# Performance work log

Measured on AMD Instinct MI355X. Metric: run time of the kernel, lower is better.

Reference implementation:

```python
import jax, jax.numpy as jnp
import numpy as np

N_NODES = 100000
K_HOPS = 10
ALPHA = 0.1


def gcn_conv(x, src, dst, W, b, num_nodes):
    # GCNConv: linear first (cheaper: out_dim small), then D^-1/2 (A+I) D^-1/2 aggregation
    h = x @ W  # [N, out]
    deg = jax.ops.segment_sum(jnp.ones_like(dst, dtype=h.dtype), dst, num_segments=num_nodes)
    dinv = jnp.where(deg > 0, jax.lax.rsqrt(deg), 0.0)
    norm = dinv[src] * dinv[dst]  # [E]
    msg = h[src] * norm[:, None]
    out = jax.ops.segment_sum(msg, dst, num_segments=num_nodes)
    return out + b


def _with_self_loops(edge_index, num_nodes):
    loops = jnp.arange(num_nodes, dtype=edge_index.dtype)
    src = jnp.concatenate([edge_index[0], loops])
    dst = jnp.concatenate([edge_index[1], loops])
    return src, dst


def setup_inputs() -> dict:
    key = jax.random.key(0)
    ks = jax.random.split(key, 8)
    n_feat, hidden, n_cls, n_edges = 512, 16, 7, 3200000
    x = jax.random.normal(ks[0], (N_NODES, n_feat), dtype=jnp.float32)
    edge_index = jax.random.randint(ks[1], (2, n_edges), 0, N_NODES, dtype=jnp.int64)
    W1 = jax.random.normal(ks[2], (n_feat, hidden), dtype=jnp.float32) * 0.05
    b1 = jnp.zeros((hidden,), dtype=jnp.float32)
    Wl = jax.random.normal(ks[3], (hidden, hidden), dtype=jnp.float32) * 0.25
    bl = jnp.zeros((hidden,), dtype=jnp.float32)
    W2 = jax.random.normal(ks[4], (hidden, n_cls), dtype=jnp.float32) * 0.25
    b2 = jnp.zeros((n_cls,), dtype=jnp.float32)
    return {"x": x, "edge_index": edge_index, "W1": W1, "b1": b1, "Wl": Wl, "bl": bl, "W2": W2, "b2": b2}


def reference(x, edge_index, W1, b1, Wl, bl, W2, b2):
    src, dst = _with_self_loops(edge_index, N_NODES)
    h = jax.nn.relu(gcn_conv(x, src, dst, W1, b1, N_NODES))
    def body(h, _):
        h = ALPHA * jax.nn.relu(h @ Wl + bl) + (1.0 - ALPHA) * h
        return h, None
    h, _ = jax.lax.scan(body, h, None, length=K_HOPS)
    out = gcn_conv(h, src, dst, W2, b2, N_NODES)
    return jax.nn.log_softmax(out, axis=1)
```

## Files before the change

### kernel.cpp

```cpp
#include <hip/hip_runtime.h>
#include <math.h>

#define N_NODES 100000
#define N_EDGES 3200000
#define F_IN    512
#define HID     16
#define NCLS    7
#define ALPHA   0.1f
#define K_HOPS  10

#define SHIFT   7
#define BWIDTH  128
#define NBUCK   ((N_NODES + BWIDTH - 1) / BWIDTH)
#define CHUNK   8192
#define A3_BLOCKS ((N_EDGES + CHUNK - 1) / CHUNK)

#define OFF_BCNT    0u
#define OFF_BSTART  1024u
#define OFF_BCUR    2048u
#define OFF_RP      3072u
#define OFF_DINV    103424u
#define OFF_COL     203776u
#define OFF_BINNED  3403776u
#define OFF_H0      3403776u
#define OFF_H1      5003776u
#define OFF_Z       6603776u

__global__ void k_bhist(const int* __restrict__ dst, int* __restrict__ bcnt) {
    __shared__ int h[NBUCK];
    int tid = threadIdx.x;
    for (int i = tid; i < NBUCK; i += 256) h[i] = 0;
    __syncthreads();
    for (int e = blockIdx.x * 256 + tid; e < N_EDGES; e += gridDim.x * 256)
        atomicAdd(&h[dst[e] >> SHIFT], 1);
    __syncthreads();
    for (int i = tid; i < NBUCK; i += 256) {
        int v = h[i];
        if (v) atomicAdd(&bcnt[i], v);
    }
}

__global__ void k_bscan(const int* __restrict__ bcnt, int* __restrict__ bstart,
                        int* __restrict__ bcur) {
    __shared__ int s[1024];
    int tid = threadIdx.x;
    int v = (tid < NBUCK) ? bcnt[tid] : 0;
    s[tid] = v;
    __syncthreads();
    for (int off = 1; off < 1024; off <<= 1) {
        int t = (tid >= off) ? s[tid - off] : 0;
        __syncthreads();
        s[tid] += t;
        __syncthreads();
    }
    if (tid < NBUCK) {
        int ex = s[tid] - v;
        bstart[tid] = ex;
        bcur[tid] = ex;
    }
    if (tid == 0) bstart[NBUCK] = N_EDGES;
}

__global__ void k_bin(const int* __restrict__ src, const int* __restrict__ dst,
                      int* __restrict__ bcur, unsigned int* __restrict__ binned) {
    __shared__ int ha[1024];
    __shared__ int hb[1024];
    __shared__ int gbase[NBUCK];
    __shared__ int lcur[NBUCK];
    int tid = threadIdx.x;
    int e0 = blockIdx.x * CHUNK;
    int e1 = e0 + CHUNK;
    if (e1 > N_EDGES) e1 = N_EDGES;
    for (int i = tid; i < 1024; i += 256) ha[i] = 0;
    __syncthreads();
    for (int e = e0 + tid; e < e1; e += 256)
        atomicAdd(&ha[dst[e] >> SHIFT], 1);
    __syncthreads();
    int* a = ha;
    int* b = hb;
    for (int off = 1; off < 1024; off <<= 1) {
        for (int s = tid; s < 1024; s += 256)
            b[s] = a[s] + ((s >= off) ? a[s - off] : 0);
        __syncthreads();
        int* t = a; a = b; b = t;
    }
    for (int s = tid; s < NBUCK; s += 256) {
        int c = a[s] - ((s > 0) ? a[s - 1] : 0);
        lcur[s] = 0;
        gbase[s] = c ? atomicAdd(&bcur[s], c) : 0;
    }
    __syncthreads();
    for (int e = e0 + tid; e < e1; e += 256) {
        int d = dst[e];
        int bk = d >> SHIFT;
        int idx = atomicAdd(&lcur[bk], 1);
        binned[gbase[bk] + idx] =
            ((unsigned int)(d & (BWIDTH - 1)) << 17) | (unsigned int)src[e];
    }
}

__global__ void k_csr(const unsigned int* __restrict__ binned, const int* __restrict__ bstart,
                      int* __restrict__ rp, float* __restrict__ dinv, int* __restrict__ col) {
    __shared__ int cnt[BWIDTH];
    __shared__ int s[BWIDTH];
    __shared__ int cur[BWIDTH];
    int tid = threadIdx.x;
    int b = blockIdx.x;
    int base = b << SHIFT;
    int e0 = bstart[b], e1 = bstart[b + 1];
    if (tid < BWIDTH) cnt[tid] = 0;
    __syncthreads();
    for (int e = e0 + tid; e < e1; e += 256)
        atomicAdd(&cnt[binned[e] >> 17], 1);
    __syncthreads();
    int v = 0;
    if (tid < BWIDTH) { v = cnt[tid]; s[tid] = v; }
    __syncthreads();
    for (int off = 1; off < BWIDTH; off <<= 1) {
        int t = 0;
        if (tid < BWIDTH && tid >= off) t = s[tid - off];
        __syncthreads();
        if (tid < BWIDTH) s[tid] += t;
        __syncthreads();
    }
    if (tid < BWIDTH) {
        int ex = s[tid] - v;
        cur[tid] = ex;
        int node = base + tid;
        if (node < N_NODES) {
            rp[node] = e0 + ex;
            dinv[node] = rsqrtf((float)(v + 1));
        }
    }
    if (b == 0 && tid == 0) rp[N_NODES] = N_EDGES;
    __syncthreads();
    for (int e = e0 + tid; e < e1; e += 256) {
        unsigned int w = binned[e];
        int ln = (int)(w >> 17);
        int p = atomicAdd(&cur[ln], 1);
        col[e0 + p] = (int)(w & 0x1FFFFu);
    }
}

#define XW_ROWS 64
#define XW_KT   32
#define XW_S    65
#define XW_NT   (F_IN / XW_KT)
__global__ void k_xw1(const float* __restrict__ x, const float* __restrict__ W,
                      const float* __restrict__ dinv, float* __restrict__ h0s) {
    __shared__ float xT[2][XW_KT * XW_S];
    int tid = threadIdx.x;
    int rowBase = blockIdx.x * XW_ROWS;

    int rf0 = tid >> 3, kq = tid & 7;
    int rf1 = rf0 + 32;
    bool v0 = (rowBase + rf0) < N_NODES;
    bool v1 = (rowBase + rf1) < N_NODES;
    const float* xrow0 = x + (size_t)(rowBase + rf0) * F_IN;
    const float* xrow1 = x + (size_t)(rowBase + rf1) * F_IN;

    int r  = tid & 63;
    int cg = __builtin_amdgcn_readfirstlane(tid >> 6);
    const float4* W4 = (const float4*)W;

    float4 zero4 = make_float4(0.f, 0.f, 0.f, 0.f);
    float4 acc = zero4;
    float4 ld0 = v0 ? ((const float4*)xrow0)[kq] : zero4;
    float4 ld1 = v1 ? ((const float4*)xrow1)[kq] : zero4;

    for (int kt = 0; kt < XW_NT; kt++) {
        int buf = kt & 1;
        float* xb = xT[buf];
        int kb = kq * 4;
        xb[(kb + 0) * XW_S + rf0] = ld0.x;
        xb[(kb + 1) * XW_S + rf0] = ld0.y;
        xb[(kb + 2) * XW_S + rf0] = ld0.z;
        xb[(kb + 3) * XW_S + rf0] = ld0.w;
        xb[(kb + 0) * XW_S + rf1] = ld1.x;
        xb[(kb + 1) * XW_S + rf1] = ld1.y;
        xb[(kb + 2) * XW_S + rf1] = ld1.z;
        xb[(kb + 3) * XW_S + rf1] = ld1.w;
        if (kt + 1 < XW_NT) {
            const float4* p0 = (const float4*)(xrow0 + (kt + 1) * XW_KT);
            const float4* p1 = (const float4*)(xrow1 + (kt + 1) * XW_KT);
            ld0 = v0 ? p0[kq] : zero4;
            ld1 = v1 ? p1[kq] : zero4;
        }
        __syncthreads();
        const float* xr = &xb[r];
#pragma unroll
        for (int k = 0; k < XW_KT; k++) {
            float xv = xr[k * XW_S];
            float4 w4 = W4[(kt * XW_KT + k) * 4 + cg];
            acc.x += xv * w4.x;
            acc.y += xv * w4.y;
            acc.z += xv * w4.z;
            acc.w += xv * w4.w;
        }
    }
    int node = rowBase + r;
    if (node < N_NODES) {
        float dv = dinv[node];
        float4 o;
        o.x = dv * acc.x; o.y = dv * acc.y; o.z = dv * acc.z; o.w = dv * acc.w;
        ((float4*)h0s)[(size_t)node * 4 + cg] = o;
    }
}

__global__ void k_agg1(const float* __restrict__ h0s, const int* __restrict__ rp,
                       const int* __restrict__ col, const float* __restrict__ dinv,
                       const float* __restrict__ b1, float* __restrict__ h1) {
    int node = (blockIdx.x * blockDim.x + threadIdx.x) >> 6;
    if (node >= N_NODES) return;
    int lane = threadIdx.x & 63;
    int c = lane & 15, eo = lane >> 4;
    int e0 = rp[node], e1 = rp[node + 1];
    float acc = 0.f;
    for (int e = e0 + eo; e < e1; e += 4)
        acc += h0s[(size_t)col[e] * HID + c];
    acc += __shfl_xor(acc, 16);
    acc += __shfl_xor(acc, 32);
    float o = dinv[node] * (acc + h0s[(size_t)node * HID + c]) + b1[c];
    if (eo == 0) h1[(size_t)node * HID + c] = fmaxf(o, 0.f);
}

__global__ void k_hops(const float* __restrict__ h1, const float* __restrict__ Wl,
                       const float* __restrict__ bl, const float* __restrict__ W2,
                       const float* __restrict__ dinv, float* __restrict__ zs) {
    int node = blockIdx.x * blockDim.x + threadIdx.x;
    if (node >= N_NODES) return;
    float h[HID];
    const float4* h4 = (const float4*)(h1 + (size_t)node * HID);
#pragma unroll
    for (int q = 0; q < HID / 4; q++) {
        float4 v = h4[q];
        h[q * 4 + 0] = v.x; h[q * 4 + 1] = v.y;
        h[q * 4 + 2] = v.z; h[q * 4 + 3] = v.w;
    }
    for (int it = 0; it < K_HOPS; it++) {
        float tm[HID];
#pragma unroll
        for (int c = 0; c < HID; c++) tm[c] = bl[c];
#pragma unroll
        for (int k = 0; k < HID; k++) {
            float hk = h[k];
#pragma unroll
            for (int c = 0; c < HID; c++) tm[c] += hk * Wl[k * HID + c];
        }
#pragma unroll
        for (int c = 0; c < HID; c++)
            h[c] = ALPHA * fmaxf(tm[c], 0.f) + (1.f - ALPHA) * h[c];
    }
    float dv = dinv[node];
    float zz[8];
#pragma unroll
    for (int c = 0; c < 8; c++) zz[c] = 0.f;
#pragma unroll
    for (int k = 0; k < HID; k++) {
        float hk = h[k];
#pragma unroll
        for (int c = 0; c < NCLS; c++) zz[c] += hk * W2[k * NCLS + c];
    }
    float4* z4 = (float4*)(zs + (size_t)node * 8);
    float4 v0, v1;
    v0.x = dv * zz[0]; v0.y = dv * zz[1]; v0.z = dv * zz[2]; v0.w = dv * zz[3];
    v1.x = dv * zz[4]; v1.y = dv * zz[5]; v1.z = dv * zz[6]; v1.w = 0.f;
    z4[0] = v0; z4[1] = v1;
}

__global__ void k_agg2(const float* __restrict__ zs, const int* __restrict__ rp,
                       const int* __restrict__ col, const float* __restrict__ dinv,
                       const float* __restrict__ b2, float* __restrict__ out) {
    int node = (blockIdx.x * blockDim.x + threadIdx.x) >> 6;
    if (node >= N_NODES) return;
    int lane = threadIdx.x & 63;
    int c = lane & 7, eo = lane >> 3;
    int e0 = rp[node], e1 = rp[node + 1];
    float acc = 0.f;
    for (int e = e0 + eo; e < e1; e += 8)
        acc += zs[(size_t)col[e] * 8 + c];
    acc += __shfl_xor(acc, 8);
    acc += __shfl_xor(acc, 16);
    acc += __shfl_xor(acc, 32);
    float o = dinv[node] * (acc + zs[(size_t)node * 8 + c]) + ((c < NCLS) ? b2[c] : 0.f);
    float val = (c < NCLS) ? o : -INFINITY;
    float m = val;
    m = fmaxf(m, __shfl_xor(m, 1));
    m = fmaxf(m, __shfl_xor(m, 2));
    m = fmaxf(m, __shfl_xor(m, 4));
    float ex = (c < NCLS) ? expf(o - m) : 0.f;
    float ss = ex;
    ss += __shfl_xor(ss, 1);
    ss += __shfl_xor(ss, 2);
    ss += __shfl_xor(ss, 4);
    if (eo == 0 && c < NCLS) out[(size_t)node * NCLS + c] = o - m - logf(ss);
}

extern "C" void kernel_launch(void* const* d_in, const int* in_sizes, int n_in,
                              void* d_out, int out_size, void* d_ws, size_t ws_size,
                              hipStream_t stream) {
    const float* x  = (const float*)d_in[0];
    const int*   ei = (const int*)d_in[1];
    const float* W1 = (const float*)d_in[2];
    const float* b1 = (const float*)d_in[3];
    const float* Wl = (const float*)d_in[4];
    const float* bl = (const float*)d_in[5];
    const float* W2 = (const float*)d_in[6];
    const float* b2 = (const float*)d_in[7];
    float* out = (float*)d_out;

    int*   wsI = (int*)d_ws;
    float* wsF = (float*)d_ws;
    int*          bcnt   = wsI + OFF_BCNT;
    int*          bstart = wsI + OFF_BSTART;
    int*          bcur   = wsI + OFF_BCUR;
    int*          rp     = wsI + OFF_RP;
    float*        dinv   = wsF + OFF_DINV;
    int*          col    = wsI + OFF_COL;
    unsigned int* binned = (unsigned int*)(wsI + OFF_BINNED);
    float*        h0s    = wsF + OFF_H0;
    float*        h1     = wsF + OFF_H1;
    float*        zs     = wsF + OFF_Z;

    const int* src = ei;
    const int* dst = ei + N_EDGES;

    hipMemsetAsync(bcnt, 0, NBUCK * sizeof(int), stream);

    k_bhist<<<1024, 256, 0, stream>>>(dst, bcnt);
    k_bscan<<<1, 1024, 0, stream>>>(bcnt, bstart, bcur);
    k_bin<<<A3_BLOCKS, 256, 0, stream>>>(src, dst, bcur, binned);
    k_csr<<<NBUCK, 256, 0, stream>>>(binned, bstart, rp, dinv, col);
    k_xw1<<<(N_NODES + XW_ROWS - 1) / XW_ROWS, 256, 0, stream>>>(x, W1, dinv, h0s);
    k_agg1<<<(N_NODES * 64 + 255) / 256, 256, 0, stream>>>(h0s, rp, col, dinv, b1, h1);
    k_hops<<<(N_NODES + 255) / 256, 256, 0, stream>>>(h1, Wl, bl, W2, dinv, zs);
    k_agg2<<<(N_NODES * 64 + 255) / 256, 256, 0, stream>>>(zs, rp, col, dinv, b2, out);
}
```

Baseline: 609.7 us.

## Drop full CSR build; aggregate per destination bucket with shared-memory atomics

Removes the second-level CSR construction (per-node row pointers and column array). The degree kernel now only computes dinv, and both aggregation kernels process a 128-node bucket per block, accumulating source features into a shared-memory tile with LDS atomics straight from the bucket-binned edge list. The binning kernel also caches dst values in registers and drops its 1024-entry prefix scan, since only per-bucket counts are needed. This saves one pass over the edge array and the col writes, but floating-point summation order becomes nondeterministic and LDS atomic contention on hot nodes may add cost.

Result: slower. 970.2 us (+59.1%).

```diff
diff --git a/kernel.cpp b/kernel.cpp
--- a/kernel.cpp
+++ b/kernel.cpp
@@ -13,18 +13,17 @@
 #define BWIDTH  128
 #define NBUCK   ((N_NODES + BWIDTH - 1) / BWIDTH)
 #define CHUNK   8192
+#define EPT     (CHUNK / 256)
 #define A3_BLOCKS ((N_EDGES + CHUNK - 1) / CHUNK)
 
 #define OFF_BCNT    0u
 #define OFF_BSTART  1024u
 #define OFF_BCUR    2048u
-#define OFF_RP      3072u
-#define OFF_DINV    103424u
-#define OFF_COL     203776u
-#define OFF_BINNED  3403776u
-#define OFF_H0      3403776u
-#define OFF_H1      5003776u
-#define OFF_Z       6603776u
+#define OFF_DINV    3072u
+#define OFF_BINNED  103424u
+#define OFF_H0      3303424u
+#define OFF_H1      4903424u
+#define OFF_Z       6503424u
 
 __global__ void k_bhist(const int* __restrict__ dst, int* __restrict__ bcnt) {
     __shared__ int h[NBUCK];
@@ -63,82 +62,57 @@
 
 __global__ void k_bin(const int* __restrict__ src, const int* __restrict__ dst,
                       int* __restrict__ bcur, unsigned int* __restrict__ binned) {
-    __shared__ int ha[1024];
-    __shared__ int hb[1024];
+    __shared__ int ha[NBUCK];
     __shared__ int gbase[NBUCK];
     __shared__ int lcur[NBUCK];
     int tid = threadIdx.x;
     int e0 = blockIdx.x * CHUNK;
     int e1 = e0 + CHUNK;
     if (e1 > N_EDGES) e1 = N_EDGES;
-    for (int i = tid; i < 1024; i += 256) ha[i] = 0;
-    __syncthreads();
-    for (int e = e0 + tid; e < e1; e += 256)
-        atomicAdd(&ha[dst[e] >> SHIFT], 1);
-    __syncthreads();
-    int* a = ha;
-    int* b = hb;
-    for (int off = 1; off < 1024; off <<= 1) {
-        for (int s = tid; s < 1024; s += 256)
-            b[s] = a[s] + ((s >= off) ? a[s - off] : 0);
-        __syncthreads();
-        int* t = a; a = b; b = t;
-    }
+    for (int i = tid; i < NBUCK; i += 256) ha[i] = 0;
+    __syncthreads();
+    int dloc[EPT];
+#pragma unroll
+    for (int i = 0; i < EPT; i++) {
+        int e = e0 + tid + i * 256;
+        dloc[i] = (e < e1) ? dst[e] : -1;
+        if (dloc[i] >= 0) atomicAdd(&ha[dloc[i] >> SHIFT], 1);
+    }
+    __syncthreads();
     for (int s = tid; s < NBUCK; s += 256) {
-        int c = a[s] - ((s > 0) ? a[s - 1] : 0);
+        int c = ha[s];
         lcur[s] = 0;
         gbase[s] = c ? atomicAdd(&bcur[s], c) : 0;
     }
     __syncthreads();
-    for (int e = e0 + tid; e < e1; e += 256) {
-        int d = dst[e];
-        int bk = d >> SHIFT;
-        int idx = atomicAdd(&lcur[bk], 1);
-        binned[gbase[bk] + idx] =
-            ((unsigned int)(d & (BWIDTH - 1)) << 17) | (unsigned int)src[e];
-    }
-}
-
-__global__ void k_csr(const unsigned int* __restrict__ binned, const int* __restrict__ bstart,
-                      int* __restrict__ rp, float* __restrict__ dinv, int* __restrict__ col) {
+#pragma unroll
+    for (int i = 0; i < EPT; i++) {
+        int d = dloc[i];
+        if (d >= 0) {
+            int e = e0 + tid + i * 256;
+            int bk = d >> SHIFT;
+            int idx = atomicAdd(&lcur[bk], 1);
+            binned[gbase[bk] + idx] =
+                ((unsigned int)(d & (BWIDTH - 1)) << 17) | (unsigned int)src[e];
+        }
+    }
+}
+
+__global__ void k_deg(const unsigned int* __restrict__ binned, const int* __restrict__ bstart,
+                      float* __restrict__ dinv) {
     __shared__ int cnt[BWIDTH];
-    __shared__ int s[BWIDTH];
-    __shared__ int cur[BWIDTH];
     int tid = threadIdx.x;
     int b = blockIdx.x;
     int base = b << SHIFT;
+    if (tid < BWIDTH) cnt[tid] = 0;
+    __syncthreads();
     int e0 = bstart[b], e1 = bstart[b + 1];
-    if (tid < BWIDTH) cnt[tid] = 0;
-    __syncthreads();
     for (int e = e0 + tid; e < e1; e += 256)
         atomicAdd(&cnt[binned[e] >> 17], 1);
     __syncthreads();
-    int v = 0;
-    if (tid < BWIDTH) { v = cnt[tid]; s[tid] = v; }
-    __syncthreads();
-    for (int off = 1; off < BWIDTH; off <<= 1) {
-        int t = 0;
-        if (tid < BWIDTH && tid >= off) t = s[tid - off];
-        __syncthreads();
-        if (tid < BWIDTH) s[tid] += t;
-        __syncthreads();
-    }
     if (tid < BWIDTH) {
-        int ex = s[tid] - v;
-        cur[tid] = ex;
         int node = base + tid;
-        if (node < N_NODES) {
-            rp[node] = e0 + ex;
-            dinv[node] = rsqrtf((float)(v + 1));
-        }
-    }
-    if (b == 0 && tid == 0) rp[N_NODES] = N_EDGES;
-    __syncthreads();
-    for (int e = e0 + tid; e < e1; e += 256) {
-        unsigned int w = binned[e];
-        int ln = (int)(w >> 17);
-        int p = atomicAdd(&cur[ln], 1);
-        col[e0 + p] = (int)(w & 0x1FFFFu);
+        if (node < N_NODES) dinv[node] = rsqrtf((float)(cnt[tid] + 1));
     }
 }
 
@@ -207,21 +181,36 @@
     }
 }
 
-__global__ void k_agg1(const float* __restrict__ h0s, const int* __restrict__ rp,
-                       const int* __restrict__ col, const float* __restrict__ dinv,
+__global__ void k_agg1(const float* __restrict__ h0s, const int* __restrict__ bstart,
+                       const unsigned int* __restrict__ binned, const float* __restrict__ dinv,
                        const float* __restrict__ b1, float* __restrict__ h1) {
-    int node = (blockIdx.x * blockDim.x + threadIdx.x) >> 6;
-    if (node >= N_NODES) return;
-    int lane = threadIdx.x & 63;
-    int c = lane & 15, eo = lane >> 4;
-    int e0 = rp[node], e1 = rp[node + 1];
-    float acc = 0.f;
-    for (int e = e0 + eo; e < e1; e += 4)
-        acc += h0s[(size_t)col[e] * HID + c];
-    acc += __shfl_xor(acc, 16);
-    acc += __shfl_xor(acc, 32);
-    float o = dinv[node] * (acc + h0s[(size_t)node * HID + c]) + b1[c];
-    if (eo == 0) h1[(size_t)node * HID + c] = fmaxf(o, 0.f);
+    __shared__ float acc[BWIDTH][HID + 1];
+    int tid = threadIdx.x;
+    int b = blockIdx.x;
+    int base = b << SHIFT;
+    for (int f = tid; f < BWIDTH * HID; f += 256) {
+        int r = f >> 4, c = f & 15;
+        int node = base + r;
+        acc[r][c] = (node < N_NODES) ? h0s[(size_t)node * HID + c] : 0.f;
+    }
+    __syncthreads();
+    int e0 = bstart[b], e1 = bstart[b + 1];
+    int g = tid >> 4, c = tid & 15;
+    for (int e = e0 + g; e < e1; e += 16) {
+        unsigned int w = binned[e];
+        int s  = (int)(w & 0x1FFFFu);
+        int dl = (int)(w >> 17);
+        atomicAdd(&acc[dl][c], h0s[(size_t)s * HID + c]);
+    }
+    __syncthreads();
+    for (int f = tid; f < BWIDTH * HID; f += 256) {
+        int r = f >> 4, cc = f & 15;
+        int node = base + r;
+        if (node < N_NODES) {
+            float o = dinv[node] * acc[r][cc] + b1[cc];
+            h1[(size_t)node * HID + cc] = fmaxf(o, 0.f);
+        }
+    }
 }
 
 __global__ void k_hops(const float* __restrict__ h1, const float* __restrict__ Wl,
@@ -268,32 +257,48 @@
     z4[0] = v0; z4[1] = v1;
 }
 
-__global__ void k_agg2(const float* __restrict__ zs, const int* __restrict__ rp,
-                       const int* __restrict__ col, const float* __restrict__ dinv,
+__global__ void k_agg2(const float* __restrict__ zs, const int* __restrict__ bstart,
+                       const unsigned int* __restrict__ binned, const float* __restrict__ dinv,
                        const float* __restrict__ b2, float* __restrict__ out) {
-    int node = (blockIdx.x * blockDim.x + threadIdx.x) >> 6;
-    if (node >= N_NODES) return;
-    int lane = threadIdx.x & 63;
-    int c = lane & 7, eo = lane >> 3;
-    int e0 = rp[node], e1 = rp[node + 1];
-    float acc = 0.f;
-    for (int e = e0 + eo; e < e1; e += 8)
-        acc += zs[(size_t)col[e] * 8 + c];
-    acc += __shfl_xor(acc, 8);
-    acc += __shfl_xor(acc, 16);
-    acc += __shfl_xor(acc, 32);
-    float o = dinv[node] * (acc + zs[(size_t)node * 8 + c]) + ((c < NCLS) ? b2[c] : 0.f);
-    float val = (c < NCLS) ? o : -INFINITY;
-    float m = val;
-    m = fmaxf(m, __shfl_xor(m, 1));
-    m = fmaxf(m, __shfl_xor(m, 2));
-    m = fmaxf(m, __shfl_xor(m, 4));
-    float ex = (c < NCLS) ? expf(o - m) : 0.f;
-    float ss = ex;
-    ss += __shfl_xor(ss, 1);
-    ss += __shfl_xor(ss, 2);
-    ss += __shfl_xor(ss, 4);
-    if (eo == 0 && c < NCLS) out[(size_t)node * NCLS + c] = o - m - logf(ss);
+    __shared__ float acc[BWIDTH][9];
+    int tid = threadIdx.x;
+    int b = blockIdx.x;
+    int base = b << SHIFT;
+    for (int f = tid; f < BWIDTH * 8; f += 256) {
+        int r = f >> 3, c = f & 7;
+        int node = base + r;
+        acc[r][c] = (node < N_NODES) ? zs[(size_t)node * 8 + c] : 0.f;
+    }
+    __syncthreads();
+    int e0 = bstart[b], e1 = bstart[b + 1];
+    int g = tid >> 3, c = tid & 7;
+    for (int e = e0 + g; e < e1; e += 32) {
+        unsigned int w = binned[e];
+        int s  = (int)(w & 0x1FFFFu);
+        int dl = (int)(w >> 17);
+        atomicAdd(&acc[dl][c], zs[(size_t)s * 8 + c]);
+    }
+    __syncthreads();
+#pragma unroll
+    for (int p = 0; p < 4; p++) {
+        int idx = p * 256 + tid;
+        int r = idx >> 3, cc = idx & 7;
+        int node = base + r;
+        float o = ((node < N_NODES) ? dinv[node] * acc[r][cc] : 0.f)
+                  + ((cc < NCLS) ? b2[cc] : 0.f);
+        float val = (cc < NCLS) ? o : -INFINITY;
+        float m = val;
+        m = fmaxf(m, __shfl_xor(m, 1));
+        m = fmaxf(m, __shfl_xor(m, 2));
+        m = fmaxf(m, __shfl_xor(m, 4));
+        float ex = (cc < NCLS) ? expf(o - m) : 0.f;
+        float ss = ex;
+        ss += __shfl_xor(ss, 1);
+        ss += __shfl_xor(ss, 2);
+        ss += __shfl_xor(ss, 4);
+        if (node < N_NODES && cc < NCLS)
+            out[(size_t)node * NCLS + cc] = o - m - logf(ss);
+    }
 }
 
 extern "C" void kernel_launch(void* const* d_in, const int* in_sizes, int n_in,
@@ -314,9 +319,7 @@
     int*          bcnt   = wsI + OFF_BCNT;
     int*          bstart = wsI + OFF_BSTART;
     int*          bcur   = wsI + OFF_BCUR;
-    int*          rp     = wsI + OFF_RP;
     float*        dinv   = wsF + OFF_DINV;
-    int*          col    = wsI + OFF_COL;
     unsigned int* binned = (unsigned int*)(wsI + OFF_BINNED);
     float*        h0s    = wsF + OFF_H0;
     float*        h1     = wsF + OFF_H1;
@@ -330,9 +333,9 @@
     k_bhist<<<1024, 256, 0, stream>>>(dst, bcnt);
     k_bscan<<<1, 1024, 0, stream>>>(bcnt, bstart, bcur);
     k_bin<<<A3_BLOCKS, 256, 0, stream>>>(src, dst, bcur, binned);
-    k_csr<<<NBUCK, 256, 0, stream>>>(binned, bstart, rp, dinv, col);
+    k_deg<<<NBUCK, 256, 0, stream>>>(binned, bstart, dinv);
     k_xw1<<<(N_NODES + XW_ROWS - 1) / XW_ROWS, 256, 0, stream>>>(x, W1, dinv, h0s);
-    k_agg1<<<(N_NODES * 64 + 255) / 256, 256, 0, stream>>>(h0s, rp, col, dinv, b1, h1);
+    k_agg1<<<NBUCK, 256, 0, stream>>>(h0s, bstart, binned, dinv, b1, h1);
     k_hops<<<(N_NODES + 255) / 256, 256, 0, stream>>>(h1, Wl, bl, W2, dinv, zs);
-    k_agg2<<<(N_NODES * 64 + 255) / 256, 256, 0, stream>>>(zs, rp, col, dinv, b2, out);
-}
+    k_agg2<<<NBUCK, 256, 0, stream>>>(zs, bstart, binned, dinv, b2, out);
+}
```
